# Optimization experiments

Measured on AMD Instinct MI355X. Metric: run time of the kernel, lower is better.

The kernel has to match this reference:

```python
import jax, jax.numpy as jnp
import numpy as np

DT = 1.0 / 60.0  # physics timestep
NUM_BODY = 20

# ---- quaternion helpers (xyzw convention, matching the repo) ----

def quat_from_rotvec(rv):
    # rv: [..., 3] axis-angle -> quaternion [..., 4] (x,y,z,w)
    angle = jnp.linalg.norm(rv, axis=-1, keepdims=True)
    half = 0.5 * angle
    safe = jnp.where(angle < 1e-8, 1.0, angle)
    s = jnp.where(angle < 1e-8, 0.5 - angle * angle / 48.0, jnp.sin(half) / safe)
    return jnp.concatenate([rv * s, jnp.cos(half)], axis=-1)


def flip_quat_by_w(q):
    return jnp.where(q[..., 3:4] < 0, -q, q)


def quat_to_vec6d(q):
    # first two columns of the rotation matrix, row-major flattened -> [..., 6]
    x, y, z, w = q[..., 0], q[..., 1], q[..., 2], q[..., 3]
    r00 = 1 - 2 * (y * y + z * z)
    r10 = 2 * (x * y + z * w)
    r20 = 2 * (x * z - y * w)
    r01 = 2 * (x * y - z * w)
    r11 = 1 - 2 * (x * x + z * z)
    r21 = 2 * (y * z + x * w)
    return jnp.stack([r00, r01, r10, r11, r20, r21], axis=-1)


def quat_apply(q, v):
    # rotate v [..., 3] by quaternion q [..., 4]; broadcasts over leading dims
    xyz, w = q[..., :3], q[..., 3:4]
    t = 2.0 * jnp.cross(xyz, v)
    return v + w * t + jnp.cross(xyz, t)


def quat_multiply(p, q):
    pv, pw = p[..., :3], p[..., 3:4]
    qv, qw = q[..., :3], q[..., 3:4]
    v = pw * qv + qw * pv + jnp.cross(pv, qv)
    w = pw * qw - jnp.sum(pv * qv, axis=-1, keepdims=True)
    return jnp.concatenate([v, w], axis=-1)


def quat_integrate(q, omega, dt):
    # q_{t+1} = normalize(q + 0.5*dt * (omega_quat * q))
    omega_q = jnp.concatenate([omega, jnp.zeros_like(omega[..., :1])], axis=-1)
    dq = quat_multiply(omega_q, q)
    r = q + 0.5 * dt * dq
    return r / jnp.linalg.norm(r, axis=-1, keepdims=True)


def integrate_state(state, delta, dt):
    # state: [B, NB, 13] = pos(3) | rot quat(4) | vel(3) | avel(3)
    B, NB, _ = state.shape
    pos, rot = state[..., 0:3], state[..., 3:7]
    vel, avel = state[..., 7:10], state[..., 10:13]
    root_rot = state[:, 0:1, 3:7]                       # [B, 1, 4]
    d3 = delta.reshape(B, -1, 3)                        # [B, 2*NB, 3]
    true_d = quat_apply(root_rot, d3).reshape(B, NB, 6)
    lin, ang = true_d[..., :3], true_d[..., 3:]
    next_vel = vel + lin
    next_avel = avel + ang
    next_pos = pos + next_vel * dt
    next_rot = quat_integrate(rot, next_avel, dt)
    return jnp.concatenate([next_pos, next_rot, next_vel, next_avel], axis=-1)


def setup_inputs() -> dict:
    key = jax.random.key(0)
    ks = jax.random.split(key, 12)
    B = 32768
    inp = {
        "state": jax.random.normal(ks[0], (B, NUM_BODY, 13), jnp.float32),
        "action": jax.random.normal(ks[1], (B, 57), jnp.float32),
        "n_observation": jax.random.normal(ks[2], (B, 300), jnp.float32),
        "W1": jax.random.normal(ks[3], (414, 512), jnp.float32) * 0.05,
        "b1": jax.random.normal(ks[4], (512,), jnp.float32) * 0.05,
        "W2": jax.random.normal(ks[5], (512, 512), jnp.float32) * 0.05,
        "b2": jax.random.normal(ks[6], (512,), jnp.float32) * 0.05,
        "W3": jax.random.normal(ks[7], (512, 120), jnp.float32) * 0.05,
        "b3": jax.random.normal(ks[8], (120,), jnp.float32) * 0.05,
        "delta_mean": jax.random.normal(ks[9], (120,), jnp.float32) * 0.01,
        "delta_std": jax.random.uniform(ks[10], (120,), jnp.float32) + 0.5,
    }
    return inp


def reference(state, action, n_observation, W1, b1, W2, b2, W3, b3, delta_mean, delta_std):
    B = action.shape[0]
    # action rotvecs -> quats -> 6d representation
    aq = flip_quat_by_w(quat_from_rotvec(action.reshape(-1, 3)))
    a6 = quat_to_vec6d(aq).reshape(B, -1)               # [B, 114]
    x = jnp.concatenate([n_observation, a6], axis=-1)   # [B, 414]
    h = jax.nn.relu(x @ W1 + b1)
    h = jax.nn.relu(h @ W2 + b2)
    n_delta = h @ W3 + b3                                # [B, 120]
    delta = n_delta * delta_std + delta_mean             # unnormalize
    return integrate_state(state, delta, DT)
```

## Files before the change

kernel.cpp:

```cpp
#include <hip/hip_runtime.h>
#include <hip/hip_bf16.h>
#include <math.h>

#define DT (1.0f / 60.0f)

typedef __bf16 bf16x8 __attribute__((ext_vector_type(8)));
typedef float f32x4 __attribute__((ext_vector_type(4)));

#define XSTRIDE 848
#define HSTRIDE 1040

struct __attribute__((packed)) f4u {
    float x, y, z, w;
};

__global__ __launch_bounds__(256) void prep_weights(
    const float* __restrict__ W1, const float* __restrict__ W2,
    const float* __restrict__ W3, __hip_bfloat16* __restrict__ W1p,
    __hip_bfloat16* __restrict__ W2p, __hip_bfloat16* __restrict__ W3p) {
    int idx = blockIdx.x * 256 + threadIdx.x;
    if (idx < 212992) {
        int d = idx;
        int e = d & 7, l = (d >> 3) & 63, t = d >> 9;
        int nt = t & 31, ks = t >> 5;
        int n = nt * 16 + (l & 15);
        int k = ks * 32 + (l >> 4) * 8 + e;
        W1p[d] = __float2bfloat16(k < 414 ? W1[k * 512 + n] : 0.0f);
        return;
    }
    idx -= 212992;
    if (idx < 262144) {
        int d = idx;
        int e = d & 7, l = (d >> 3) & 63, t = d >> 9;
        int nt = t & 31, ks = t >> 5;
        int n = nt * 16 + (l & 15);
        int k = ks * 32 + (l >> 4) * 8 + e;
        W2p[d] = __float2bfloat16(W2[k * 512 + n]);
        return;
    }
    idx -= 262144;
    if (idx < 65536) {
        int d = idx;
        int e = d & 7, l = (d >> 3) & 63, t = d >> 9;
        int nt = t & 7, ks = t >> 3;
        int n = nt * 16 + (l & 15);
        int k = ks * 32 + (l >> 4) * 8 + e;
        W3p[d] = __float2bfloat16(n < 120 ? W3[k * 120 + n] : 0.0f);
    }
}

template <int KSTEPS, int NT, int ASTRIDE>
__device__ __forceinline__ void mlp_layer(const char* Abase, const char* Bbase,
                                          int laneOff, f32x4 (&acc)[4][8]) {
    bf16x8 w0[8], w1[8];
#pragma unroll
    for (int j = 0; j < 8; j++)
        w0[j] = *(const bf16x8*)(Bbase + (j << 10) + laneOff);
#pragma unroll 2
    for (int ks = 0; ks < KSTEPS; ks++) {
        if (ks + 1 < KSTEPS) {
            if ((ks & 1) == 0) {
#pragma unroll
                for (int j = 0; j < 8; j++)
                    w1[j] = *(const bf16x8*)(Bbase + (((ks + 1) * NT + j) << 10) + laneOff);
            } else {
#pragma unroll
                for (int j = 0; j < 8; j++)
                    w0[j] = *(const bf16x8*)(Bbase + (((ks + 1) * NT + j) << 10) + laneOff);
            }
        }
        bf16x8 ax[4];
#pragma unroll
        for (int i = 0; i < 4; i++)
            ax[i] = *(const bf16x8*)(Abase + ks * 64 + i * 16 * ASTRIDE);
#pragma unroll
        for (int i = 0; i < 4; i++)
#pragma unroll
            for (int j = 0; j < 8; j++)
                acc[i][j] = __builtin_amdgcn_mfma_f32_16x16x32_bf16(
                    (ks & 1) ? w1[j] : w0[j], ax[i], acc[i][j], 0, 0, 0);
    }
}

__device__ __forceinline__ void store_h_relu_t(const f32x4 (&acc)[4][8],
                                               char* smem, const float* bias,
                                               int wn, int lrow, int kgrp) {
#pragma unroll
    for (int j = 0; j < 8; j++) {
        int f = wn * 128 + j * 16 + kgrp * 4;
        float4 bb = *(const float4*)(bias + f);
#pragma unroll
        for (int i = 0; i < 4; i++) {
            float v0 = acc[i][j][0] + bb.x;
            float v1 = acc[i][j][1] + bb.y;
            float v2 = acc[i][j][2] + bb.z;
            float v3 = acc[i][j][3] + bb.w;
            v0 = v0 > 0.0f ? v0 : 0.0f;
            v1 = v1 > 0.0f ? v1 : 0.0f;
            v2 = v2 > 0.0f ? v2 : 0.0f;
            v3 = v3 > 0.0f ? v3 : 0.0f;
            union { __hip_bfloat162 h2[2]; uint2 u; } pk;
            pk.h2[0] = __float22bfloat162_rn(make_float2(v0, v1));
            pk.h2[1] = __float22bfloat162_rn(make_float2(v2, v3));
            *(uint2*)(smem + (i * 16 + lrow) * HSTRIDE + f * 2) = pk.u;
        }
    }
}

__device__ __forceinline__ void quat_apply3(float qx, float qy, float qz,
                                            float qw, float vx, float vy,
                                            float vz, float& ox, float& oy,
                                            float& oz) {
    float tx = 2.0f * (qy * vz - qz * vy);
    float ty = 2.0f * (qz * vx - qx * vz);
    float tz = 2.0f * (qx * vy - qy * vx);
    ox = vx + qw * tx + (qy * tz - qz * ty);
    oy = vy + qw * ty + (qz * tx - qx * tz);
    oz = vz + qw * tz + (qx * ty - qy * tx);
}

__global__ __launch_bounds__(256, 2) void fused_mlp(
    const float* __restrict__ obs, const float* __restrict__ action,
    const __hip_bfloat16* __restrict__ W1p, const float* __restrict__ b1,
    const __hip_bfloat16* __restrict__ W2p, const float* __restrict__ b2,
    const __hip_bfloat16* __restrict__ W3p, const float* __restrict__ b3,
    const float* __restrict__ dstd, const float* __restrict__ dmean,
    const float* __restrict__ state, float* __restrict__ out) {
    alignas(16) __shared__ char smem[64 * HSTRIDE];
    const int tid = threadIdx.x;
    const int blk = blockIdx.x;
    const int lane = tid & 63, wn = tid >> 6;
    const int lrow = lane & 15, kgrp = lane >> 4;
    const int laneOff = lane * 16;

    {
        const float4* og = (const float4*)obs + (size_t)blk * 64 * 75;
#pragma unroll
        for (int i = 0; i < 19; i++) {
            int f = tid + i * 256;
            if (f < 4800) {
                int row = f / 75;
                int c4 = f - row * 75;
                float4 v = og[f];
                union { __hip_bfloat162 h2[2]; uint2 u; } pk;
                pk.h2[0] = __float22bfloat162_rn(make_float2(v.x, v.y));
                pk.h2[1] = __float22bfloat162_rn(make_float2(v.z, v.w));
                *(uint2*)(smem + row * XSTRIDE + c4 * 8) = pk.u;
            }
        }
#pragma unroll
        for (int i = 0; i < 5; i++) {
            int q = tid + i * 256;
            if (q < 1216) {
                int row = q / 19;
                int j = q - row * 19;
                const float* a = action + ((size_t)(blk * 64 + row)) * 57 + j * 3;
                float rx = a[0], ry = a[1], rz = a[2];
                float ang = sqrtf(rx * rx + ry * ry + rz * rz);
                float half = 0.5f * ang;
                float s;
                if (ang < 1e-8f)
                    s = 0.5f - ang * ang * (1.0f / 48.0f);
                else
                    s = sinf(half) / ang;
                float qx = rx * s, qy = ry * s, qz = rz * s, qw = cosf(half);
                union { __hip_bfloat16 h[6]; uint u[3]; } pq;
                pq.h[0] = __float2bfloat16(1.0f - 2.0f * (qy * qy + qz * qz));
                pq.h[1] = __float2bfloat16(2.0f * (qx * qy - qz * qw));
                pq.h[2] = __float2bfloat16(2.0f * (qx * qy + qz * qw));
                pq.h[3] = __float2bfloat16(1.0f - 2.0f * (qx * qx + qz * qz));
                pq.h[4] = __float2bfloat16(2.0f * (qx * qz - qy * qw));
                pq.h[5] = __float2bfloat16(2.0f * (qy * qz + qx * qw));
                char* p = smem + row * XSTRIDE + 600 + j * 12;
                *(uint*)p = pq.u[0];
                *(uint*)(p + 4) = pq.u[1];
                *(uint*)(p + 8) = pq.u[2];
            }
        }
#pragma unroll
        for (int i = 0; i < 2; i++) {
            int id = tid + i * 256;
            if (id < 320) {
                int row = id / 5;
                int p = id - row * 5;
                *(uint*)(smem + row * XSTRIDE + 828 + p * 4) = 0u;
            }
        }
    }
    __syncthreads();

    f32x4 acc[4][8];
    f32x4 zero4 = {0.0f, 0.0f, 0.0f, 0.0f};
#pragma unroll
    for (int i = 0; i < 4; i++)
#pragma unroll
        for (int j = 0; j < 8; j++) acc[i][j] = zero4;

    mlp_layer<13, 32, XSTRIDE>(smem + lrow * XSTRIDE + kgrp * 16,
                               (const char*)W1p + (wn << 13), laneOff, acc);
    __syncthreads();
    store_h_relu_t(acc, smem, b1, wn, lrow, kgrp);
    __syncthreads();

#pragma unroll
    for (int i = 0; i < 4; i++)
#pragma unroll
        for (int j = 0; j < 8; j++) acc[i][j] = zero4;
    mlp_layer<16, 32, HSTRIDE>(smem + lrow * HSTRIDE + kgrp * 16,
                               (const char*)W2p + (wn << 13), laneOff, acc);
    __syncthreads();
    store_h_relu_t(acc, smem, b2, wn, lrow, kgrp);
    __syncthreads();

    f4u ps0[5], ps1[5], ps2[5], prq[5];
    float ps12[5];
#pragma unroll
    for (int it = 0; it < 5; it++) {
        int idx = tid + it * 256;
        int lr = idx / 20;
        int body = idx - lr * 20;
        const float* sb = state + ((size_t)(blk * 64 + lr)) * 260 + body * 13;
        const float* rq = state + ((size_t)(blk * 64 + lr)) * 260 + 3;
        ps0[it] = *(const f4u*)sb;
        ps1[it] = *(const f4u*)(sb + 4);
        ps2[it] = *(const f4u*)(sb + 8);
        ps12[it] = sb[12];
        prq[it] = *(const f4u*)rq;
    }

    f32x4 a3[4][2];
#pragma unroll
    for (int i = 0; i < 4; i++)
#pragma unroll
        for (int j = 0; j < 2; j++) a3[i][j] = zero4;
    {
        const char* Ab = smem + lrow * HSTRIDE + kgrp * 16;
        const char* Bb = (const char*)W3p;
        bf16x8 c0[2], c1[2];
#pragma unroll
        for (int j = 0; j < 2; j++)
            c0[j] = *(const bf16x8*)(Bb + ((wn * 2 + j) << 10) + laneOff);
#pragma unroll 2
        for (int ks = 0; ks < 16; ks++) {
            if (ks + 1 < 16) {
                if ((ks & 1) == 0) {
#pragma unroll
                    for (int j = 0; j < 2; j++)
                        c1[j] = *(const bf16x8*)(Bb + (((ks + 1) * 8 + wn * 2 + j) << 10) + laneOff);
                } else {
#pragma unroll
                    for (int j = 0; j < 2; j++)
                        c0[j] = *(const bf16x8*)(Bb + (((ks + 1) * 8 + wn * 2 + j) << 10) + laneOff);
                }
            }
            bf16x8 ax[4];
#pragma unroll
            for (int i = 0; i < 4; i++)
                ax[i] = *(const bf16x8*)(Ab + ks * 64 + i * 16 * HSTRIDE);
#pragma unroll
            for (int i = 0; i < 4; i++)
#pragma unroll
                for (int j = 0; j < 2; j++)
                    a3[i][j] = __builtin_amdgcn_mfma_f32_16x16x32_bf16(
                        (ks & 1) ? c1[j] : c0[j], ax[i], a3[i][j], 0, 0, 0);
        }
    }
    __syncthreads();

    float* dl = (float*)smem;
#pragma unroll
    for (int j = 0; j < 2; j++) {
        int f = wn * 32 + j * 16 + kgrp * 4;
        if (f < 120) {
            float4 bb = *(const float4*)(b3 + f);
            float4 sc = *(const float4*)(dstd + f);
            float4 mn = *(const float4*)(dmean + f);
#pragma unroll
            for (int i = 0; i < 4; i++) {
                int row = i * 16 + lrow;
                float4 dv;
                dv.x = (a3[i][j][0] + bb.x) * sc.x + mn.x;
                dv.y = (a3[i][j][1] + bb.y) * sc.y + mn.y;
                dv.z = (a3[i][j][2] + bb.z) * sc.z + mn.z;
                dv.w = (a3[i][j][3] + bb.w) * sc.w + mn.w;
                *(float4*)(dl + row * 120 + f) = dv;
            }
        }
    }
    __syncthreads();

#pragma unroll
    for (int it = 0; it < 5; it++) {
        int idx = tid + it * 256;
        int lr = idx / 20;
        int body = idx - lr * 20;
        int rowg = blk * 64 + lr;
        float qx = prq[it].x, qy = prq[it].y, qz = prq[it].z, qw = prq[it].w;
        const float* d = dl + lr * 120 + body * 6;

        float lx, ly, lz, ax, ay, az;
        quat_apply3(qx, qy, qz, qw, d[0], d[1], d[2], lx, ly, lz);
        quat_apply3(qx, qy, qz, qw, d[3], d[4], d[5], ax, ay, az);

        float vx = ps1[it].w + lx, vy = ps2[it].x + ly, vz = ps2[it].y + lz;
        float wx = ps2[it].z + ax, wy = ps2[it].w + ay, wz = ps12[it] + az;
        float px = ps0[it].x + vx * DT, py = ps0[it].y + vy * DT,
              pz = ps0[it].z + vz * DT;

        float rx = ps0[it].w, ry = ps1[it].x, rz = ps1[it].y, rw = ps1[it].z;
        float dqx = rw * wx + (wy * rz - wz * ry);
        float dqy = rw * wy + (wz * rx - wx * rz);
        float dqz = rw * wz + (wx * ry - wy * rx);
        float dqw = -(wx * rx + wy * ry + wz * rz);
        float h = 0.5f * DT;
        float nx = rx + h * dqx, ny = ry + h * dqy, nz = rz + h * dqz,
              nw = rw + h * dqw;
        float inv = 1.0f / sqrtf(nx * nx + ny * ny + nz * nz + nw * nw);

        float* o = out + (size_t)rowg * 260 + body * 13;
        o[0] = px;
        o[1] = py;
        o[2] = pz;
        o[3] = nx * inv;
        o[4] = ny * inv;
        o[5] = nz * inv;
        o[6] = nw * inv;
        o[7] = vx;
        o[8] = vy;
        o[9] = vz;
        o[10] = wx;
        o[11] = wy;
        o[12] = wz;
    }
}

extern "C" void kernel_launch(void* const* d_in, const int* in_sizes, int n_in,
                              void* d_out, int out_size, void* d_ws,
                              size_t ws_size, hipStream_t stream) {
    const float* state = (const float*)d_in[0];
    const float* action = (const float*)d_in[1];
    const float* obs = (const float*)d_in[2];
    const float* W1 = (const float*)d_in[3];
    const float* b1 = (const float*)d_in[4];
    const float* W2 = (const float*)d_in[5];
    const float* b2 = (const float*)d_in[6];
    const float* W3 = (const float*)d_in[7];
    const float* b3 = (const float*)d_in[8];
    const float* dmean = (const float*)d_in[9];
    const float* dstd = (const float*)d_in[10];
    float* out = (float*)d_out;
    char* ws = (char*)d_ws;

    const int B = in_sizes[1] / 57;

    __hip_bfloat16* W1p = (__hip_bfloat16*)(ws);
    __hip_bfloat16* W2p = (__hip_bfloat16*)(ws + 425984);
    __hip_bfloat16* W3p = (__hip_bfloat16*)(ws + 950272);

    prep_weights<<<2112, 256, 0, stream>>>(W1, W2, W3, W1p, W2p, W3p);
    fused_mlp<<<B / 64, 256, 0, stream>>>(obs, action, W1p, b1, W2p, b2, W3p,
                                          b3, dstd, dmean, state, out);
}
```

Before: 165.7 us.

## Split MLP output columns across 8 waves per block instead of 4

The fused MLP kernel moves from 256 to 512 threads per block. Each of 8 waves now computes 64 output columns (4 MFMA tiles) rather than 128, and layer 3 uses one 16-column tile per wave. Prologue loads, state loads and the integration epilogue are redistributed over 512 threads. This halves per-wave accumulator and weight-register pressure and adds waves for latency hiding. In exchange, each wave re-reads the same activation rows from LDS, so LDS traffic per block doubles, and barriers now span more waves.

```diff
diff --git a/kernel.cpp b/kernel.cpp
--- a/kernel.cpp
+++ b/kernel.cpp
@@ -49,23 +49,23 @@
     }
 }
 
-template <int KSTEPS, int NT, int ASTRIDE>
+template <int KSTEPS, int NT, int JF, int ASTRIDE>
 __device__ __forceinline__ void mlp_layer(const char* Abase, const char* Bbase,
-                                          int laneOff, f32x4 (&acc)[4][8]) {
-    bf16x8 w0[8], w1[8];
-#pragma unroll
-    for (int j = 0; j < 8; j++)
+                                          int laneOff, f32x4 (&acc)[4][JF]) {
+    bf16x8 w0[JF], w1[JF];
+#pragma unroll
+    for (int j = 0; j < JF; j++)
         w0[j] = *(const bf16x8*)(Bbase + (j << 10) + laneOff);
 #pragma unroll 2
     for (int ks = 0; ks < KSTEPS; ks++) {
         if (ks + 1 < KSTEPS) {
             if ((ks & 1) == 0) {
 #pragma unroll
-                for (int j = 0; j < 8; j++)
+                for (int j = 0; j < JF; j++)
                     w1[j] = *(const bf16x8*)(Bbase + (((ks + 1) * NT + j) << 10) + laneOff);
             } else {
 #pragma unroll
-                for (int j = 0; j < 8; j++)
+                for (int j = 0; j < JF; j++)
                     w0[j] = *(const bf16x8*)(Bbase + (((ks + 1) * NT + j) << 10) + laneOff);
             }
         }
@@ -76,18 +76,18 @@
 #pragma unroll
         for (int i = 0; i < 4; i++)
 #pragma unroll
-            for (int j = 0; j < 8; j++)
+            for (int j = 0; j < JF; j++)
                 acc[i][j] = __builtin_amdgcn_mfma_f32_16x16x32_bf16(
                     (ks & 1) ? w1[j] : w0[j], ax[i], acc[i][j], 0, 0, 0);
     }
 }
 
-__device__ __forceinline__ void store_h_relu_t(const f32x4 (&acc)[4][8],
+__device__ __forceinline__ void store_h_relu_t(const f32x4 (&acc)[4][4],
                                                char* smem, const float* bias,
                                                int wn, int lrow, int kgrp) {
 #pragma unroll
-    for (int j = 0; j < 8; j++) {
-        int f = wn * 128 + j * 16 + kgrp * 4;
+    for (int j = 0; j < 4; j++) {
+        int f = wn * 64 + j * 16 + kgrp * 4;
         float4 bb = *(const float4*)(bias + f);
 #pragma unroll
         for (int i = 0; i < 4; i++) {
@@ -119,7 +119,7 @@
     oz = vz + qw * tz + (qx * ty - qy * tx);
 }
 
-__global__ __launch_bounds__(256, 2) void fused_mlp(
+__global__ __launch_bounds__(512, 4) void fused_mlp(
     const float* __restrict__ obs, const float* __restrict__ action,
     const __hip_bfloat16* __restrict__ W1p, const float* __restrict__ b1,
     const __hip_bfloat16* __restrict__ W2p, const float* __restrict__ b2,
@@ -136,8 +136,8 @@
     {
         const float4* og = (const float4*)obs + (size_t)blk * 64 * 75;
 #pragma unroll
-        for (int i = 0; i < 19; i++) {
-            int f = tid + i * 256;
+        for (int i = 0; i < 10; i++) {
+            int f = tid + i * 512;
             if (f < 4800) {
                 int row = f / 75;
                 int c4 = f - row * 75;
@@ -149,8 +149,8 @@
             }
         }
 #pragma unroll
-        for (int i = 0; i < 5; i++) {
-            int q = tid + i * 256;
+        for (int i = 0; i < 3; i++) {
+            int q = tid + i * 512;
             if (q < 1216) {
                 int row = q / 19;
                 int j = q - row * 19;
@@ -177,27 +177,23 @@
                 *(uint*)(p + 8) = pq.u[2];
             }
         }
-#pragma unroll
-        for (int i = 0; i < 2; i++) {
-            int id = tid + i * 256;
-            if (id < 320) {
-                int row = id / 5;
-                int p = id - row * 5;
-                *(uint*)(smem + row * XSTRIDE + 828 + p * 4) = 0u;
-            }
-        }
-    }
-    __syncthreads();
-
-    f32x4 acc[4][8];
+        if (tid < 320) {
+            int row = tid / 5;
+            int p = tid - row * 5;
+            *(uint*)(smem + row * XSTRIDE + 828 + p * 4) = 0u;
+        }
+    }
+    __syncthreads();
+
+    f32x4 acc[4][4];
     f32x4 zero4 = {0.0f, 0.0f, 0.0f, 0.0f};
 #pragma unroll
     for (int i = 0; i < 4; i++)
 #pragma unroll
-        for (int j = 0; j < 8; j++) acc[i][j] = zero4;
-
-    mlp_layer<13, 32, XSTRIDE>(smem + lrow * XSTRIDE + kgrp * 16,
-                               (const char*)W1p + (wn << 13), laneOff, acc);
+        for (int j = 0; j < 4; j++) acc[i][j] = zero4;
+
+    mlp_layer<13, 32, 4, XSTRIDE>(smem + lrow * XSTRIDE + kgrp * 16,
+                                  (const char*)W1p + (wn << 12), laneOff, acc);
     __syncthreads();
     store_h_relu_t(acc, smem, b1, wn, lrow, kgrp);
     __syncthreads();
@@ -205,53 +201,46 @@
 #pragma unroll
     for (int i = 0; i < 4; i++)
 #pragma unroll
-        for (int j = 0; j < 8; j++) acc[i][j] = zero4;
-    mlp_layer<16, 32, HSTRIDE>(smem + lrow * HSTRIDE + kgrp * 16,
-                               (const char*)W2p + (wn << 13), laneOff, acc);
+        for (int j = 0; j < 4; j++) acc[i][j] = zero4;
+    mlp_layer<16, 32, 4, HSTRIDE>(smem + lrow * HSTRIDE + kgrp * 16,
+                                  (const char*)W2p + (wn << 12), laneOff, acc);
     __syncthreads();
     store_h_relu_t(acc, smem, b2, wn, lrow, kgrp);
     __syncthreads();
 
-    f4u ps0[5], ps1[5], ps2[5], prq[5];
-    float ps12[5];
-#pragma unroll
-    for (int it = 0; it < 5; it++) {
-        int idx = tid + it * 256;
-        int lr = idx / 20;
-        int body = idx - lr * 20;
-        const float* sb = state + ((size_t)(blk * 64 + lr)) * 260 + body * 13;
-        const float* rq = state + ((size_t)(blk * 64 + lr)) * 260 + 3;
-        ps0[it] = *(const f4u*)sb;
-        ps1[it] = *(const f4u*)(sb + 4);
-        ps2[it] = *(const f4u*)(sb + 8);
-        ps12[it] = sb[12];
-        prq[it] = *(const f4u*)rq;
-    }
-
-    f32x4 a3[4][2];
-#pragma unroll
-    for (int i = 0; i < 4; i++)
-#pragma unroll
-        for (int j = 0; j < 2; j++) a3[i][j] = zero4;
+    f4u ps0[3], ps1[3], ps2[3], prq[3];
+    float ps12[3];
+#pragma unroll
+    for (int it = 0; it < 3; it++) {
+        int idx = tid + it * 512;
+        if (idx < 1280) {
+            int lr = idx / 20;
+            int body = idx - lr * 20;
+            const float* sb = state + ((size_t)(blk * 64 + lr)) * 260 + body * 13;
+            const float* rq = state + ((size_t)(blk * 64 + lr)) * 260 + 3;
+            ps0[it] = *(const f4u*)sb;
+            ps1[it] = *(const f4u*)(sb + 4);
+            ps2[it] = *(const f4u*)(sb + 8);
+            ps12[it] = sb[12];
+            prq[it] = *(const f4u*)rq;
+        }
+    }
+
+    f32x4 a3[4];
+#pragma unroll
+    for (int i = 0; i < 4; i++) a3[i] = zero4;
     {
         const char* Ab = smem + lrow * HSTRIDE + kgrp * 16;
-        const char* Bb = (const char*)W3p;
-        bf16x8 c0[2], c1[2];
-#pragma unroll
-        for (int j = 0; j < 2; j++)
-            c0[j] = *(const bf16x8*)(Bb + ((wn * 2 + j) << 10) + laneOff);
+        const char* Bb = (const char*)W3p + (wn << 10);
+        bf16x8 c0 = *(const bf16x8*)(Bb + laneOff);
+        bf16x8 c1;
 #pragma unroll 2
         for (int ks = 0; ks < 16; ks++) {
             if (ks + 1 < 16) {
-                if ((ks & 1) == 0) {
-#pragma unroll
-                    for (int j = 0; j < 2; j++)
-                        c1[j] = *(const bf16x8*)(Bb + (((ks + 1) * 8 + wn * 2 + j) << 10) + laneOff);
-                } else {
-#pragma unroll
-                    for (int j = 0; j < 2; j++)
-                        c0[j] = *(const bf16x8*)(Bb + (((ks + 1) * 8 + wn * 2 + j) << 10) + laneOff);
-                }
+                if ((ks & 1) == 0)
+                    c1 = *(const bf16x8*)(Bb + ((ks + 1) << 13) + laneOff);
+                else
+                    c0 = *(const bf16x8*)(Bb + ((ks + 1) << 13) + laneOff);
             }
             bf16x8 ax[4];
 #pragma unroll
@@ -259,18 +248,15 @@
                 ax[i] = *(const bf16x8*)(Ab + ks * 64 + i * 16 * HSTRIDE);
 #pragma unroll
             for (int i = 0; i < 4; i++)
-#pragma unroll
-                for (int j = 0; j < 2; j++)
-                    a3[i][j] = __builtin_amdgcn_mfma_f32_16x16x32_bf16(
-                        (ks & 1) ? c1[j] : c0[j], ax[i], a3[i][j], 0, 0, 0);
+                a3[i] = __builtin_amdgcn_mfma_f32_16x16x32_bf16(
+                    (ks & 1) ? c1 : c0, ax[i], a3[i], 0, 0, 0);
         }
     }
     __syncthreads();
 
     float* dl = (float*)smem;
-#pragma unroll
-    for (int j = 0; j < 2; j++) {
-        int f = wn * 32 + j * 16 + kgrp * 4;
+    {
+        int f = wn * 16 + kgrp * 4;
         if (f < 120) {
             float4 bb = *(const float4*)(b3 + f);
             float4 sc = *(const float4*)(dstd + f);
@@ -279,10 +265,10 @@
             for (int i = 0; i < 4; i++) {
                 int row = i * 16 + lrow;
                 float4 dv;
-                dv.x = (a3[i][j][0] + bb.x) * sc.x + mn.x;
-                dv.y = (a3[i][j][1] + bb.y) * sc.y + mn.y;
-                dv.z = (a3[i][j][2] + bb.z) * sc.z + mn.z;
-                dv.w = (a3[i][j][3] + bb.w) * sc.w + mn.w;
+                dv.x = (a3[i][0] + bb.x) * sc.x + mn.x;
+                dv.y = (a3[i][1] + bb.y) * sc.y + mn.y;
+                dv.z = (a3[i][2] + bb.z) * sc.z + mn.z;
+                dv.w = (a3[i][3] + bb.w) * sc.w + mn.w;
                 *(float4*)(dl + row * 120 + f) = dv;
             }
         }
@@ -290,47 +276,49 @@
     __syncthreads();
 
 #pragma unroll
-    for (int it = 0; it < 5; it++) {
-        int idx = tid + it * 256;
-        int lr = idx / 20;
-        int body = idx - lr * 20;
-        int rowg = blk * 64 + lr;
-        float qx = prq[it].x, qy = prq[it].y, qz = prq[it].z, qw = prq[it].w;
-        const float* d = dl + lr * 120 + body * 6;
-
-        float lx, ly, lz, ax, ay, az;
-        quat_apply3(qx, qy, qz, qw, d[0], d[1], d[2], lx, ly, lz);
-        quat_apply3(qx, qy, qz, qw, d[3], d[4], d[5], ax, ay, az);
-
-        float vx = ps1[it].w + lx, vy = ps2[it].x + ly, vz = ps2[it].y + lz;
-        float wx = ps2[it].z + ax, wy = ps2[it].w + ay, wz = ps12[it] + az;
-        float px = ps0[it].x + vx * DT, py = ps0[it].y + vy * DT,
-              pz = ps0[it].z + vz * DT;
-
-        float rx = ps0[it].w, ry = ps1[it].x, rz = ps1[it].y, rw = ps1[it].z;
-        float dqx = rw * wx + (wy * rz - wz * ry);
-        float dqy = rw * wy + (wz * rx - wx * rz);
-        float dqz = rw * wz + (wx * ry - wy * rx);
-        float dqw = -(wx * rx + wy * ry + wz * rz);
-        float h = 0.5f * DT;
-        float nx = rx + h * dqx, ny = ry + h * dqy, nz = rz + h * dqz,
-              nw = rw + h * dqw;
-        float inv = 1.0f / sqrtf(nx * nx + ny * ny + nz * nz + nw * nw);
-
-        float* o = out + (size_t)rowg * 260 + body * 13;
-        o[0] = px;
-        o[1] = py;
-        o[2] = pz;
-        o[3] = nx * inv;
-        o[4] = ny * inv;
-        o[5] = nz * inv;
-        o[6] = nw * inv;
-        o[7] = vx;
-        o[8] = vy;
-        o[9] = vz;
-        o[10] = wx;
-        o[11] = wy;
-        o[12] = wz;
+    for (int it = 0; it < 3; it++) {
+        int idx = tid + it * 512;
+        if (idx < 1280) {
+            int lr = idx / 20;
+            int body = idx - lr * 20;
+            int rowg = blk * 64 + lr;
+            float qx = prq[it].x, qy = prq[it].y, qz = prq[it].z, qw = prq[it].w;
+            const float* d = dl + lr * 120 + body * 6;
+
+            float lx, ly, lz, ax, ay, az;
+            quat_apply3(qx, qy, qz, qw, d[0], d[1], d[2], lx, ly, lz);
+            quat_apply3(qx, qy, qz, qw, d[3], d[4], d[5], ax, ay, az);
+
+            float vx = ps1[it].w + lx, vy = ps2[it].x + ly, vz = ps2[it].y + lz;
+            float wx = ps2[it].z + ax, wy = ps2[it].w + ay, wz = ps12[it] + az;
+            float px = ps0[it].x + vx * DT, py = ps0[it].y + vy * DT,
+                  pz = ps0[it].z + vz * DT;
+
+            float rx = ps0[it].w, ry = ps1[it].x, rz = ps1[it].y, rw = ps1[it].z;
+            float dqx = rw * wx + (wy * rz - wz * ry);
+            float dqy = rw * wy + (wz * rx - wx * rz);
+            float dqz = rw * wz + (wx * ry - wy * rx);
+            float dqw = -(wx * rx + wy * ry + wz * rz);
+            float h = 0.5f * DT;
+            float nx = rx + h * dqx, ny = ry + h * dqy, nz = rz + h * dqz,
+                  nw = rw + h * dqw;
+            float inv = 1.0f / sqrtf(nx * nx + ny * ny + nz * nz + nw * nw);
+
+            float* o = out + (size_t)rowg * 260 + body * 13;
+            o[0] = px;
+            o[1] = py;
+            o[2] = pz;
+            o[3] = nx * inv;
+            o[4] = ny * inv;
+            o[5] = nz * inv;
+            o[6] = nw * inv;
+            o[7] = vx;
+            o[8] = vy;
+            o[9] = vz;
+            o[10] = wx;
+            o[11] = wy;
+            o[12] = wz;
+        }
     }
 }
 
@@ -358,6 +346,6 @@
     __hip_bfloat16* W3p = (__hip_bfloat16*)(ws + 950272);
 
     prep_weights<<<2112, 256, 0, stream>>>(W1, W2, W3, W1p, W2p, W3p);
-    fused_mlp<<<B / 64, 256, 0, stream>>>(obs, action, W1p, b1, W2p, b2, W3p,
+    fused_mlp<<<B / 64, 512, 0, stream>>>(obs, action, W1p, b1, W2p, b2, W3p,
                                           b3, dstd, dmean, state, out);
 }
```

Measured after the change: 166.9 us. About the same (+0.7%).
